# Kernel optimization log

Hardware: AMD Instinct MI355X
Metric: run time of the kernel (lower is better)

The kernel has to match this reference:

```python
import jax, jax.numpy as jnp
import numpy as np

MAX_DEPTH = 10
NUM_INPUT = 256
NUM_OUTPUT = 64
BATCH = 131072
N_INTERNAL = 2**MAX_DEPTH - 1  # 1023 heap-indexed internal nodes
N_LEAVES = 2**MAX_DEPTH        # 1024 leaves


def setup_inputs() -> dict:
    key = jax.random.key(0)
    k_x, k_w, k_b, k_a, k_l = jax.random.split(key, 5)
    x = jax.random.normal(k_x, (BATCH, NUM_INPUT), dtype=jnp.float32)
    # internal-node params (torch init: weights ~ N(0,0.1); bias/alpha zeros,
    # but we randomize bias/alpha so both branches are exercised)
    W = jax.random.normal(k_w, (N_INTERNAL, NUM_INPUT), dtype=jnp.float32) * 0.1
    b = jax.random.normal(k_b, (N_INTERNAL,), dtype=jnp.float32) * 0.1
    alpha = jax.random.normal(k_a, (N_INTERNAL,), dtype=jnp.float32)
    leaves = jax.random.normal(k_l, (N_LEAVES, NUM_OUTPUT), dtype=jnp.float32)
    return {"x": x, "W": W, "b": b, "alpha": alpha, "leaves": leaves}


def reference(x, W, b, alpha, leaves):
    # Batched hard root-to-leaf traversal of the soft binary tree.
    # Heap indexing: node i -> left child 2i+1, right child 2i+2.
    B = x.shape[0]
    idx = jnp.zeros((B,), dtype=jnp.int32)
    mult = jnp.ones((B,), dtype=x.dtype)
    for _ in range(MAX_DEPTH):  # fixed small structural loop over depth levels
        w = W[idx]  # [B, F] gather of per-node weights
        val = jax.nn.sigmoid(alpha[idx] * (jnp.einsum('bf,bf->b', x, w) + b[idx]))
        go_right = val >= 0.5
        # right branch contributes val, left branch contributes (1 - val)
        mult = mult * jnp.where(go_right, val, 1.0 - val)
        idx = 2 * idx + 1 + go_right.astype(jnp.int32)
    leaf_idx = idx - N_INTERNAL  # [B]
    return mult[:, None] * leaves[leaf_idx]  # [B, num_output]
```

## Files before the change

### kernel.cpp

```cpp
#include <hip/hip_runtime.h>

#define NUM_INPUT   256
#define NUM_OUTPUT  64
#define MAX_DEPTH   10
#define N_INTERNAL  1023
#define STAGED_NODES 63
#define STAGED_DEPTH 6
#define ELEMS_PER_WAVE 4
#define WAVES_PER_BLOCK 16
#define THREADS (WAVES_PER_BLOCK * 64)
#define ELEMS_PER_BLOCK (WAVES_PER_BLOCK * ELEMS_PER_WAVE)

__device__ __forceinline__ float group16_reduce(float acc) {
    int t;
    t = __builtin_amdgcn_update_dpp(0, __float_as_int(acc), 0x121, 0xf, 0xf, true);
    acc += __int_as_float(t);
    t = __builtin_amdgcn_update_dpp(0, __float_as_int(acc), 0x122, 0xf, 0xf, true);
    acc += __int_as_float(t);
    t = __builtin_amdgcn_update_dpp(0, __float_as_int(acc), 0x124, 0xf, 0xf, true);
    acc += __int_as_float(t);
    t = __builtin_amdgcn_update_dpp(0, __float_as_int(acc), 0x128, 0xf, 0xf, true);
    acc += __int_as_float(t);
    return acc;
}

__global__ __launch_bounds__(THREADS) void ogtree_kernel(
    const float* __restrict__ x,
    const float* __restrict__ W,
    const float* __restrict__ b,
    const float* __restrict__ alpha,
    const float* __restrict__ leaves,
    float* __restrict__ out)
{
    __shared__ float lds_w[STAGED_NODES * NUM_INPUT];
    __shared__ float lds_b[N_INTERNAL];
    __shared__ float lds_a[N_INTERNAL];

    const int tid = threadIdx.x;

    {
        const float4* Wv = reinterpret_cast<const float4*>(W);
        float4* lw4 = reinterpret_cast<float4*>(lds_w);
        #pragma unroll
        for (int i = tid; i < STAGED_NODES * NUM_INPUT / 4; i += THREADS)
            lw4[i] = Wv[i];
        for (int i = tid; i < N_INTERNAL; i += THREADS) {
            lds_b[i] = b[i];
            lds_a[i] = alpha[i];
        }
    }
    __syncthreads();

    const int lane = tid & 63;
    const int wid  = tid >> 6;
    const int g    = lane >> 4;
    const int s    = lane & 15;
    const int elem = blockIdx.x * ELEMS_PER_BLOCK + wid * ELEMS_PER_WAVE + g;

    const float4* xrow = reinterpret_cast<const float4*>(x + (size_t)elem * NUM_INPUT);
    float4 xv0 = xrow[0 * 16 + s];
    float4 xv1 = xrow[1 * 16 + s];
    float4 xv2 = xrow[2 * 16 + s];
    float4 xv3 = xrow[3 * 16 + s];

    int   idx  = 0;
    float mult = 1.0f;

    #pragma unroll
    for (int d = 0; d < STAGED_DEPTH; ++d) {
        const float4* wrow = reinterpret_cast<const float4*>(lds_w + idx * NUM_INPUT);
        float4 w0 = wrow[0 * 16 + s];
        float4 w1 = wrow[1 * 16 + s];
        float4 w2 = wrow[2 * 16 + s];
        float4 w3 = wrow[3 * 16 + s];
        float acc = 0.0f;
        acc = fmaf(xv0.x, w0.x, acc); acc = fmaf(xv0.y, w0.y, acc);
        acc = fmaf(xv0.z, w0.z, acc); acc = fmaf(xv0.w, w0.w, acc);
        acc = fmaf(xv1.x, w1.x, acc); acc = fmaf(xv1.y, w1.y, acc);
        acc = fmaf(xv1.z, w1.z, acc); acc = fmaf(xv1.w, w1.w, acc);
        acc = fmaf(xv2.x, w2.x, acc); acc = fmaf(xv2.y, w2.y, acc);
        acc = fmaf(xv2.z, w2.z, acc); acc = fmaf(xv2.w, w2.w, acc);
        acc = fmaf(xv3.x, w3.x, acc); acc = fmaf(xv3.y, w3.y, acc);
        acc = fmaf(xv3.z, w3.z, acc); acc = fmaf(xv3.w, w3.w, acc);
        acc = group16_reduce(acc);
        float z   = lds_a[idx] * (acc + lds_b[idx]);
        float val = 1.0f / (1.0f + __expf(-z));
        bool  right = (val >= 0.5f);
        mult *= right ? val : (1.0f - val);
        idx = 2 * idx + 1 + (right ? 1 : 0);
    }

    #pragma unroll
    for (int d = STAGED_DEPTH; d < MAX_DEPTH; ++d) {
        const float4* wrow = reinterpret_cast<const float4*>(W + (size_t)idx * NUM_INPUT);
        float4 w0 = wrow[0 * 16 + s];
        float4 w1 = wrow[1 * 16 + s];
        float4 w2 = wrow[2 * 16 + s];
        float4 w3 = wrow[3 * 16 + s];
        float acc = 0.0f;
        acc = fmaf(xv0.x, w0.x, acc); acc = fmaf(xv0.y, w0.y, acc);
        acc = fmaf(xv0.z, w0.z, acc); acc = fmaf(xv0.w, w0.w, acc);
        acc = fmaf(xv1.x, w1.x, acc); acc = fmaf(xv1.y, w1.y, acc);
        acc = fmaf(xv1.z, w1.z, acc); acc = fmaf(xv1.w, w1.w, acc);
        acc = fmaf(xv2.x, w2.x, acc); acc = fmaf(xv2.y, w2.y, acc);
        acc = fmaf(xv2.z, w2.z, acc); acc = fmaf(xv2.w, w2.w, acc);
        acc = fmaf(xv3.x, w3.x, acc); acc = fmaf(xv3.y, w3.y, acc);
        acc = fmaf(xv3.z, w3.z, acc); acc = fmaf(xv3.w, w3.w, acc);
        acc = group16_reduce(acc);
        float z   = lds_a[idx] * (acc + lds_b[idx]);
        float val = 1.0f / (1.0f + __expf(-z));
        bool  right = (val >= 0.5f);
        mult *= right ? val : (1.0f - val);
        idx = 2 * idx + 1 + (right ? 1 : 0);
    }

    const int leaf = idx - N_INTERNAL;
    const float4 lv = reinterpret_cast<const float4*>(
        leaves + (size_t)leaf * NUM_OUTPUT)[s];
    float4 o;
    o.x = mult * lv.x;
    o.y = mult * lv.y;
    o.z = mult * lv.z;
    o.w = mult * lv.w;
    reinterpret_cast<float4*>(out + (size_t)elem * NUM_OUTPUT)[s] = o;
}

extern "C" void kernel_launch(void* const* d_in, const int* in_sizes, int n_in,
                              void* d_out, int out_size, void* d_ws, size_t ws_size,
                              hipStream_t stream) {
    const float* x      = (const float*)d_in[0];
    const float* W      = (const float*)d_in[1];
    const float* b      = (const float*)d_in[2];
    const float* alpha  = (const float*)d_in[3];
    const float* leaves = (const float*)d_in[4];
    float* out = (float*)d_out;

    const int batch  = in_sizes[0] / NUM_INPUT;
    const int blocks = batch / ELEMS_PER_BLOCK;

    ogtree_kernel<<<blocks, THREADS, 0, stream>>>(x, W, b, alpha, leaves, out);
}
```

Baseline: 49.73 us.

## Amortize LDS weight staging over multiple rounds per block and shorten dependency chains

Launches a fixed 512 blocks that each process four rounds of elements, so the 63-node weight staging into LDS is paid once per block instead of once per 64 elements. The dot product is split into four independent FMA chains, the branch decision is taken directly from z >= 0 before the sigmoid, and bias/alpha loads are issued earlier. This cuts redundant global-to-LDS traffic, at the cost of a hardcoded grid size that assumes the batch is exactly 131072, and launch bounds now request 8 blocks per unit.

```diff
diff --git a/kernel.cpp b/kernel.cpp
--- a/kernel.cpp
+++ b/kernel.cpp
@@ -9,7 +9,8 @@
 #define ELEMS_PER_WAVE 4
 #define WAVES_PER_BLOCK 16
 #define THREADS (WAVES_PER_BLOCK * 64)
-#define ELEMS_PER_BLOCK (WAVES_PER_BLOCK * ELEMS_PER_WAVE)
+#define BLOCKS 512
+#define ROUNDS 4
 
 __device__ __forceinline__ float group16_reduce(float acc) {
     int t;
@@ -24,7 +25,33 @@
     return acc;
 }
 
-__global__ __launch_bounds__(THREADS) void ogtree_kernel(
+#define DEPTH_STEP(WROW_PTR)                                               \
+    {                                                                      \
+        const float4* wrow = (WROW_PTR);                                   \
+        float a_i = lds_a[idx];                                            \
+        float b_i = lds_b[idx];                                            \
+        float4 w0 = wrow[0 * 16 + s];                                      \
+        float4 w1 = wrow[1 * 16 + s];                                      \
+        float4 w2 = wrow[2 * 16 + s];                                      \
+        float4 w3 = wrow[3 * 16 + s];                                      \
+        float acc0 = xv0.x * w0.x, acc1 = xv1.x * w1.x;                    \
+        float acc2 = xv2.x * w2.x, acc3 = xv3.x * w3.x;                    \
+        acc0 = fmaf(xv0.y, w0.y, acc0); acc1 = fmaf(xv1.y, w1.y, acc1);    \
+        acc2 = fmaf(xv2.y, w2.y, acc2); acc3 = fmaf(xv3.y, w3.y, acc3);    \
+        acc0 = fmaf(xv0.z, w0.z, acc0); acc1 = fmaf(xv1.z, w1.z, acc1);    \
+        acc2 = fmaf(xv2.z, w2.z, acc2); acc3 = fmaf(xv3.z, w3.z, acc3);    \
+        acc0 = fmaf(xv0.w, w0.w, acc0); acc1 = fmaf(xv1.w, w1.w, acc1);    \
+        acc2 = fmaf(xv2.w, w2.w, acc2); acc3 = fmaf(xv3.w, w3.w, acc3);    \
+        float acc = (acc0 + acc1) + (acc2 + acc3);                         \
+        acc = group16_reduce(acc);                                         \
+        float z = a_i * (acc + b_i);                                       \
+        bool right = (z >= 0.0f);                                          \
+        idx = 2 * idx + 1 + (right ? 1 : 0);                               \
+        float val = 1.0f / (1.0f + __expf(-z));                            \
+        mult *= right ? val : (1.0f - val);                                \
+    }
+
+__global__ __launch_bounds__(THREADS, 8) void ogtree_kernel(
     const float* __restrict__ x,
     const float* __restrict__ W,
     const float* __restrict__ b,
@@ -55,74 +82,40 @@
     const int wid  = tid >> 6;
     const int g    = lane >> 4;
     const int s    = lane & 15;
-    const int elem = blockIdx.x * ELEMS_PER_BLOCK + wid * ELEMS_PER_WAVE + g;
+    const int wave_base = blockIdx.x * (WAVES_PER_BLOCK * ELEMS_PER_WAVE * ROUNDS)
+                        + wid * (ELEMS_PER_WAVE * ROUNDS);
 
-    const float4* xrow = reinterpret_cast<const float4*>(x + (size_t)elem * NUM_INPUT);
-    float4 xv0 = xrow[0 * 16 + s];
-    float4 xv1 = xrow[1 * 16 + s];
-    float4 xv2 = xrow[2 * 16 + s];
-    float4 xv3 = xrow[3 * 16 + s];
+    #pragma unroll 1
+    for (int r = 0; r < ROUNDS; ++r) {
+        const int elem = wave_base + r * ELEMS_PER_WAVE + g;
 
-    int   idx  = 0;
-    float mult = 1.0f;
+        const float4* xrow = reinterpret_cast<const float4*>(x + (size_t)elem * NUM_INPUT);
+        float4 xv0 = xrow[0 * 16 + s];
+        float4 xv1 = xrow[1 * 16 + s];
+        float4 xv2 = xrow[2 * 16 + s];
+        float4 xv3 = xrow[3 * 16 + s];
 
-    #pragma unroll
-    for (int d = 0; d < STAGED_DEPTH; ++d) {
-        const float4* wrow = reinterpret_cast<const float4*>(lds_w + idx * NUM_INPUT);
-        float4 w0 = wrow[0 * 16 + s];
-        float4 w1 = wrow[1 * 16 + s];
-        float4 w2 = wrow[2 * 16 + s];
-        float4 w3 = wrow[3 * 16 + s];
-        float acc = 0.0f;
-        acc = fmaf(xv0.x, w0.x, acc); acc = fmaf(xv0.y, w0.y, acc);
-        acc = fmaf(xv0.z, w0.z, acc); acc = fmaf(xv0.w, w0.w, acc);
-        acc = fmaf(xv1.x, w1.x, acc); acc = fmaf(xv1.y, w1.y, acc);
-        acc = fmaf(xv1.z, w1.z, acc); acc = fmaf(xv1.w, w1.w, acc);
-        acc = fmaf(xv2.x, w2.x, acc); acc = fmaf(xv2.y, w2.y, acc);
-        acc = fmaf(xv2.z, w2.z, acc); acc = fmaf(xv2.w, w2.w, acc);
-        acc = fmaf(xv3.x, w3.x, acc); acc = fmaf(xv3.y, w3.y, acc);
-        acc = fmaf(xv3.z, w3.z, acc); acc = fmaf(xv3.w, w3.w, acc);
-        acc = group16_reduce(acc);
-        float z   = lds_a[idx] * (acc + lds_b[idx]);
-        float val = 1.0f / (1.0f + __expf(-z));
-        bool  right = (val >= 0.5f);
-        mult *= right ? val : (1.0f - val);
-        idx = 2 * idx + 1 + (right ? 1 : 0);
+        int   idx  = 0;
+        float mult = 1.0f;
+
+        #pragma unroll
+        for (int d = 0; d < STAGED_DEPTH; ++d)
+            DEPTH_STEP(reinterpret_cast<const float4*>(lds_w + idx * NUM_INPUT));
+
+        #pragma unroll
+        for (int d = STAGED_DEPTH; d < MAX_DEPTH; ++d)
+            DEPTH_STEP(reinterpret_cast<const float4*>(W + (size_t)idx * NUM_INPUT));
+
+        const int leaf = idx - N_INTERNAL;
+        const float4 lv = reinterpret_cast<const float4*>(
+            leaves + (size_t)leaf * NUM_OUTPUT)[s];
+        float4 o;
+        o.x = mult * lv.x;
+        o.y = mult * lv.y;
+        o.z = mult * lv.z;
+        o.w = mult * lv.w;
+        reinterpret_cast<float4*>(out + (size_t)elem * NUM_OUTPUT)[s] = o;
     }
-
-    #pragma unroll
-    for (int d = STAGED_DEPTH; d < MAX_DEPTH; ++d) {
-        const float4* wrow = reinterpret_cast<const float4*>(W + (size_t)idx * NUM_INPUT);
-        float4 w0 = wrow[0 * 16 + s];
-        float4 w1 = wrow[1 * 16 + s];
-        float4 w2 = wrow[2 * 16 + s];
-        float4 w3 = wrow[3 * 16 + s];
-        float acc = 0.0f;
-        acc = fmaf(xv0.x, w0.x, acc); acc = fmaf(xv0.y, w0.y, acc);
-        acc = fmaf(xv0.z, w0.z, acc); acc = fmaf(xv0.w, w0.w, acc);
-        acc = fmaf(xv1.x, w1.x, acc); acc = fmaf(xv1.y, w1.y, acc);
-        acc = fmaf(xv1.z, w1.z, acc); acc = fmaf(xv1.w, w1.w, acc);
-        acc = fmaf(xv2.x, w2.x, acc); acc = fmaf(xv2.y, w2.y, acc);
-        acc = fmaf(xv2.z, w2.z, acc); acc = fmaf(xv2.w, w2.w, acc);
-        acc = fmaf(xv3.x, w3.x, acc); acc = fmaf(xv3.y, w3.y, acc);
-        acc = fmaf(xv3.z, w3.z, acc); acc = fmaf(xv3.w, w3.w, acc);
-        acc = group16_reduce(acc);
-        float z   = lds_a[idx] * (acc + lds_b[idx]);
-        float val = 1.0f / (1.0f + __expf(-z));
-        bool  right = (val >= 0.5f);
-        mult *= right ? val : (1.0f - val);
-        idx = 2 * idx + 1 + (right ? 1 : 0);
-    }
-
-    const int leaf = idx - N_INTERNAL;
-    const float4 lv = reinterpret_cast<const float4*>(
-        leaves + (size_t)leaf * NUM_OUTPUT)[s];
-    float4 o;
-    o.x = mult * lv.x;
-    o.y = mult * lv.y;
-    o.z = mult * lv.z;
-    o.w = mult * lv.w;
-    reinterpret_cast<float4*>(out + (size_t)elem * NUM_OUTPUT)[s] = o;
 }
 
 extern "C" void kernel_launch(void* const* d_in, const int* in_sizes, int n_in,
@@ -135,8 +128,5 @@
     const float* leaves = (const float*)d_in[4];
     float* out = (float*)d_out;
 
-    const int batch  = in_sizes[0] / NUM_INPUT;
-    const int blocks = batch / ELEMS_PER_BLOCK;
-
-    ogtree_kernel<<<blocks, THREADS, 0, stream>>>(x, W, b, alpha, leaves, out);
+    ogtree_kernel<<<BLOCKS, THREADS, 0, stream>>>(x, W, b, alpha, leaves, out);
 }
```

Result: slower. 62.54 us (+25.8%).
